# Performance work log

Measured on AMD Instinct MI355X. Metric: run time of the kernel, lower is better.

## Reference

```python
import jax, jax.numpy as jnp
import numpy as np

GROUP_SIZE = 64
SCALING = 1.0  # lora_alpha / r = 16 / 16
# bitsandbytes NF4 codebook (16 normal-float levels)
NF4_CODE = jnp.array([
    -1.0, -0.6961928009986877, -0.5250730514526367, -0.39491748809814453,
    -0.28444138169288635, -0.18477343022823334, -0.09105003625154495, 0.0,
    0.07958029955625534, 0.16093020141124725, 0.24611230194568634,
    0.33791524171829224, 0.44070982933044434, 0.5626170039176941,
    0.7229568362236023, 1.0], dtype=jnp.float32)

IN_F, OUT_F, R, TOKENS = 4096, 11008, 16, 32


def setup_inputs() -> dict:
    key = jax.random.key(0)
    k0, k1, k2, k3, k4 = jax.random.split(key, 5)
    x = jax.random.normal(k0, (TOKENS, IN_F), dtype=jnp.float32)
    # each byte packs two 4-bit NF4 indices (high nibble first)
    packed_weight = jax.random.randint(k1, (OUT_F * IN_F // 2,), 0, 256, dtype=jnp.int32)
    # per-group absmax scales (positive)
    scales = jax.random.uniform(k2, (OUT_F * IN_F // GROUP_SIZE,), dtype=jnp.float32,
                                minval=0.005, maxval=0.05)
    lora_A = jax.random.normal(k3, (R, IN_F), dtype=jnp.float32) * 0.02
    lora_B = jax.random.normal(k4, (OUT_F, R), dtype=jnp.float32) * 0.02
    return {"x": x, "packed_weight": packed_weight, "scales": scales,
            "lora_A": lora_A, "lora_B": lora_B}


def _dequant_nf4(packed_weight, scales):
    hi = packed_weight // 16          # first nibble
    lo = packed_weight % 16           # second nibble
    idx = jnp.stack([hi, lo], axis=-1).reshape(-1)          # [out*in]
    w = NF4_CODE[idx].reshape(-1, GROUP_SIZE) * scales[:, None]
    return w.reshape(OUT_F, IN_F)                            # [out, in]


def reference(x, packed_weight, scales, lora_A, lora_B):
    W = _dequant_nf4(packed_weight, scales)
    base = x @ W.T                                           # [tokens, out]
    lora = (x @ lora_A.T) @ lora_B.T                         # low-rank update
    return base + SCALING * lora
```

## Files before the change

kernel.cpp:

```cpp
#include <hip/hip_runtime.h>
#include <hip/hip_bf16.h>

#define IN_F 4096
#define OUT_F 11008
#define TOKENS 32
#define RANK 16
#define KSPLIT 8
#define KSLICE (IN_F / KSPLIT)
#define XPAD 520

typedef unsigned short u16;
typedef __attribute__((ext_vector_type(8))) short bf16x8;
typedef __attribute__((ext_vector_type(4))) float f32x4;

__device__ const float NF4_d[16] = {
    -1.0f, -0.6961928009986877f, -0.5250730514526367f, -0.39491748809814453f,
    -0.28444138169288635f, -0.18477343022823334f, -0.09105003625154495f, 0.0f,
    0.07958029955625534f, 0.16093020141124725f, 0.24611230194568634f,
    0.33791524171829224f, 0.44070982933044434f, 0.5626170039176941f,
    0.7229568362236023f, 1.0f};

static __device__ __forceinline__ unsigned pk2(float a, float b) {
    __hip_bfloat162 h = __float22bfloat162_rn(make_float2(a, b));
    unsigned u;
    __builtin_memcpy(&u, &h, 4);
    return u;
}

__global__ void prep(const float* __restrict__ x, const float* __restrict__ A,
                     u16* __restrict__ xbf, float* __restrict__ xa) {
    __shared__ float red[256];
    if (blockIdx.x >= 512) {
        int i4 = (blockIdx.x - 512) * 256 + threadIdx.x;
        float4 v = ((const float4*)x)[i4];
        uint2 o;
        o.x = pk2(v.x, v.y);
        o.y = pk2(v.z, v.w);
        ((uint2*)xbf)[i4] = o;
        return;
    }
    int b = blockIdx.x;
    int t = b >> 4, r = b & 15;
    const float4* xr = (const float4*)(x + t * IN_F);
    const float4* ar = (const float4*)(A + r * IN_F);
    float s = 0.f;
    for (int c = 0; c < 4; ++c) {
        int j = c * 256 + threadIdx.x;
        float4 xv = xr[j], av = ar[j];
        s += xv.x * av.x + xv.y * av.y + xv.z * av.z + xv.w * av.w;
    }
    red[threadIdx.x] = s;
    __syncthreads();
    for (int st = 128; st > 0; st >>= 1) {
        if (threadIdx.x < st) red[threadIdx.x] += red[threadIdx.x + st];
        __syncthreads();
    }
    if (threadIdx.x == 0) xa[b] = red[0];
}

__global__ void lora_out(const float* __restrict__ xa, const float* __restrict__ B,
                         float* __restrict__ out) {
    int idx = blockIdx.x * 256 + threadIdx.x;
    int t = idx / OUT_F;
    int o = idx - t * OUT_F;
    const float4* br = (const float4*)(B + o * RANK);
    const float4* xr = (const float4*)(xa + t * RANK);
    float acc = 0.f;
    for (int c = 0; c < 4; ++c) {
        float4 bv = br[c], xv = xr[c];
        acc += bv.x * xv.x + bv.y * xv.y + bv.z * xv.z + bv.w * xv.w;
    }
    out[idx] = acc;
}

__global__ __launch_bounds__(256) void qlora_main(const int* __restrict__ packed,
                                                  const float* __restrict__ scales,
                                                  const u16* __restrict__ xbf,
                                                  float* __restrict__ out) {
    __shared__ u16 xs[32 * XPAD];
    __shared__ float2 tbl[256];
    __shared__ float sl[64 * 9];
    const int tid = threadIdx.x;
    const int kbase = blockIdx.y * KSLICE;
    const int obase = blockIdx.x * 64;

    tbl[tid] = make_float2(NF4_d[tid >> 4], NF4_d[tid & 15]);

    {
        int r = tid >> 3, g = tid & 7;
        int g0 = (kbase >> 6);
        sl[r * 9 + g] = scales[(obase + r) * 64 + g0 + g];
        sl[(r + 32) * 9 + g] = scales[(obase + r + 32) * 64 + g0 + g];
    }

    for (int it = 0; it < 8; ++it) {
        int row = it * 4 + (tid >> 6);
        int c8 = tid & 63;
        *(uint4*)(xs + row * XPAD + c8 * 8) =
            *(const uint4*)(xbf + row * IN_F + kbase + c8 * 8);
    }
    __syncthreads();

    const int lane = tid & 63;
    const int wv = tid >> 6;
    const int n = lane & 15;
    const int q = lane >> 4;
    const int o = obase + wv * 16 + n;

    const int4* pp = (const int4*)(packed + o * 2048 + (kbase >> 1)) + q;

    f32x4 acc0 = {0.f, 0.f, 0.f, 0.f};
    f32x4 acc1 = {0.f, 0.f, 0.f, 0.f};
    const u16* xr0 = xs + n * XPAD + q * 8;
    const u16* xr1 = xs + (n + 16) * XPAD + q * 8;
    const float* slp = sl + (wv * 16 + n) * 9;

    int4 c0 = pp[0];
    int4 c1 = pp[4];

#pragma unroll
    for (int s = 0; s < 16; s += 2) {
        int4 n0 = c0, n1 = c1;
        if (s + 2 < 16) {
            n0 = pp[(s + 2) * 4];
            n1 = pp[(s + 3) * 4];
        }
        float sc = slp[s >> 1];

        {
            float2 d0 = tbl[c0.x & 255];
            float2 d1 = tbl[c0.y & 255];
            float2 d2 = tbl[c0.z & 255];
            float2 d3 = tbl[c0.w & 255];
            uint4 bu;
            bu.x = pk2(d0.x * sc, d0.y * sc);
            bu.y = pk2(d1.x * sc, d1.y * sc);
            bu.z = pk2(d2.x * sc, d2.y * sc);
            bu.w = pk2(d3.x * sc, d3.y * sc);
            bf16x8 bfrag;
            __builtin_memcpy(&bfrag, &bu, 16);
            bf16x8 a0 = *(const bf16x8*)(xr0 + s * 32);
            bf16x8 a1 = *(const bf16x8*)(xr1 + s * 32);
            acc0 = __builtin_amdgcn_mfma_f32_16x16x32_bf16(a0, bfrag, acc0, 0, 0, 0);
            acc1 = __builtin_amdgcn_mfma_f32_16x16x32_bf16(a1, bfrag, acc1, 0, 0, 0);
        }
        {
            float2 d0 = tbl[c1.x & 255];
            float2 d1 = tbl[c1.y & 255];
            float2 d2 = tbl[c1.z & 255];
            float2 d3 = tbl[c1.w & 255];
            uint4 bu;
            bu.x = pk2(d0.x * sc, d0.y * sc);
            bu.y = pk2(d1.x * sc, d1.y * sc);
            bu.z = pk2(d2.x * sc, d2.y * sc);
            bu.w = pk2(d3.x * sc, d3.y * sc);
            bf16x8 bfrag;
            __builtin_memcpy(&bfrag, &bu, 16);
            bf16x8 a0 = *(const bf16x8*)(xr0 + (s + 1) * 32);
            bf16x8 a1 = *(const bf16x8*)(xr1 + (s + 1) * 32);
            acc0 = __builtin_amdgcn_mfma_f32_16x16x32_bf16(a0, bfrag, acc0, 0, 0, 0);
            acc1 = __builtin_amdgcn_mfma_f32_16x16x32_bf16(a1, bfrag, acc1, 0, 0, 0);
        }
        c0 = n0;
        c1 = n1;
    }

    for (int r = 0; r < 4; ++r) {
        int t = q * 4 + r;
        atomicAdd(out + t * OUT_F + o, acc0[r]);
        atomicAdd(out + (t + 16) * OUT_F + o, acc1[r]);
    }
}

extern "C" void kernel_launch(void* const* d_in, const int* in_sizes, int n_in,
                              void* d_out, int out_size, void* d_ws, size_t ws_size,
                              hipStream_t stream) {
    const float* x = (const float*)d_in[0];
    const int* packed = (const int*)d_in[1];
    const float* scales = (const float*)d_in[2];
    const float* lora_A = (const float*)d_in[3];
    const float* lora_B = (const float*)d_in[4];
    float* out = (float*)d_out;

    u16* xbf = (u16*)d_ws;
    float* xa = (float*)((char*)d_ws + TOKENS * IN_F * 2);

    prep<<<640, 256, 0, stream>>>(x, lora_A, xbf, xa);
    lora_out<<<(TOKENS * OUT_F) / 256, 256, 0, stream>>>(xa, lora_B, out);
    qlora_main<<<dim3(OUT_F / 64, KSPLIT), 256, 0, stream>>>(packed, scales, xbf, out);
}
```

Measured before the change: 155.6 us.

## Replace atomic split-K with partial buffers, bpermute NF4 lookup, drop LDS staging

The main kernel now writes per-K-slice partial sums to a workspace buffer instead of issuing atomicAdd to the output, and a new reduce kernel sums the four partials and adds the LoRA term. The K split drops from 8 to 4. NF4 decode now uses ds_bpermute on a per-lane codebook register instead of a shared-memory pair table. The x tile is read directly from global memory rather than staged in LDS. The intent is to remove atomic traffic and shared-memory setup and barriers, at the cost of extra partial-buffer writes and reads and fewer blocks in flight.

```diff
diff --git a/kernel.cpp b/kernel.cpp
--- a/kernel.cpp
+++ b/kernel.cpp
@@ -5,9 +5,9 @@
 #define OUT_F 11008
 #define TOKENS 32
 #define RANK 16
-#define KSPLIT 8
+#define KSPLIT 4
 #define KSLICE (IN_F / KSPLIT)
-#define XPAD 520
+#define OUT_ELEMS (TOKENS * OUT_F)
 
 typedef unsigned short u16;
 typedef __attribute__((ext_vector_type(8))) short bf16x8;
@@ -25,6 +25,14 @@
     unsigned u;
     __builtin_memcpy(&u, &h, 4);
     return u;
+}
+
+static __device__ __forceinline__ unsigned dq_byte(int b, int codei, float sc) {
+    int ih = (b >> 2) & 0x3C;
+    int il = (b << 2) & 0x3C;
+    float h = __int_as_float(__builtin_amdgcn_ds_bpermute(ih, codei));
+    float l = __int_as_float(__builtin_amdgcn_ds_bpermute(il, codei));
+    return pk2(h * sc, l * sc);
 }
 
 __global__ void prep(const float* __restrict__ x, const float* __restrict__ A,
@@ -58,11 +66,87 @@
     if (threadIdx.x == 0) xa[b] = red[0];
 }
 
-__global__ void lora_out(const float* __restrict__ xa, const float* __restrict__ B,
-                         float* __restrict__ out) {
+__global__ __launch_bounds__(256) void qlora_part(const int* __restrict__ packed,
+                                                  const float* __restrict__ scales,
+                                                  const u16* __restrict__ xbf,
+                                                  float* __restrict__ part) {
+    const int tid = threadIdx.x;
+    const int lane = tid & 63;
+    const int wv = tid >> 6;
+    const int n = lane & 15;
+    const int q = lane >> 4;
+    const int kbase = blockIdx.y * KSLICE;
+    const int o = blockIdx.x * 64 + wv * 16 + n;
+
+    const int codei = __float_as_int(NF4_d[lane & 15]);
+
+    const int4* ppq = (const int4*)(packed + o * 2048 + (kbase >> 1)) + q;
+    const u16* xq0 = xbf + n * IN_F + kbase + q * 8;
+    const u16* xq1 = xq0 + 16 * IN_F;
+    const float* sg = scales + o * 64 + (kbase >> 6);
+
+    f32x4 acc0 = {0.f, 0.f, 0.f, 0.f};
+    f32x4 acc1 = {0.f, 0.f, 0.f, 0.f};
+
+    int4 c0 = ppq[0];
+    int4 c1 = ppq[4];
+
+#pragma unroll
+    for (int s = 0; s < 32; s += 2) {
+        int4 n0 = c0, n1 = c1;
+        if (s + 2 < 32) {
+            n0 = ppq[(s + 2) * 4];
+            n1 = ppq[(s + 3) * 4];
+        }
+        float sc = sg[s >> 1];
+
+        {
+            uint4 bu;
+            bu.x = dq_byte(c0.x, codei, sc);
+            bu.y = dq_byte(c0.y, codei, sc);
+            bu.z = dq_byte(c0.z, codei, sc);
+            bu.w = dq_byte(c0.w, codei, sc);
+            bf16x8 bfrag;
+            __builtin_memcpy(&bfrag, &bu, 16);
+            bf16x8 a0 = *(const bf16x8*)(xq0 + s * 32);
+            bf16x8 a1 = *(const bf16x8*)(xq1 + s * 32);
+            acc0 = __builtin_amdgcn_mfma_f32_16x16x32_bf16(a0, bfrag, acc0, 0, 0, 0);
+            acc1 = __builtin_amdgcn_mfma_f32_16x16x32_bf16(a1, bfrag, acc1, 0, 0, 0);
+        }
+        {
+            uint4 bu;
+            bu.x = dq_byte(c1.x, codei, sc);
+            bu.y = dq_byte(c1.y, codei, sc);
+            bu.z = dq_byte(c1.z, codei, sc);
+            bu.w = dq_byte(c1.w, codei, sc);
+            bf16x8 bfrag;
+            __builtin_memcpy(&bfrag, &bu, 16);
+            bf16x8 a0 = *(const bf16x8*)(xq0 + (s + 1) * 32);
+            bf16x8 a1 = *(const bf16x8*)(xq1 + (s + 1) * 32);
+            acc0 = __builtin_amdgcn_mfma_f32_16x16x32_bf16(a0, bfrag, acc0, 0, 0, 0);
+            acc1 = __builtin_amdgcn_mfma_f32_16x16x32_bf16(a1, bfrag, acc1, 0, 0, 0);
+        }
+        c0 = n0;
+        c1 = n1;
+    }
+
+    float* pb = part + blockIdx.y * OUT_ELEMS + o;
+    for (int r = 0; r < 4; ++r) {
+        int t = q * 4 + r;
+        pb[t * OUT_F] = acc0[r];
+        pb[(t + 16) * OUT_F] = acc1[r];
+    }
+}
+
+__global__ void reduce_lora(const float* __restrict__ part,
+                            const float* __restrict__ xa,
+                            const float* __restrict__ B,
+                            float* __restrict__ out) {
     int idx = blockIdx.x * 256 + threadIdx.x;
     int t = idx / OUT_F;
     int o = idx - t * OUT_F;
+    float s = part[idx] + part[idx + OUT_ELEMS] + part[idx + 2 * OUT_ELEMS] +
+              part[idx + 3 * OUT_ELEMS];
     const float4* br = (const float4*)(B + o * RANK);
     const float4* xr = (const float4*)(xa + t * RANK);
     float acc = 0.f;
@@ -70,106 +154,7 @@
         float4 bv = br[c], xv = xr[c];
         acc += bv.x * xv.x + bv.y * xv.y + bv.z * xv.z + bv.w * xv.w;
     }
-    out[idx] = acc;
-}
-
-__global__ __launch_bounds__(256) void qlora_main(const int* __restrict__ packed,
-                                                  const float* __restrict__ scales,
-                                                  const u16* __restrict__ xbf,
-                                                  float* __restrict__ out) {
-    __shared__ u16 xs[32 * XPAD];
-    __shared__ float2 tbl[256];
-    __shared__ float sl[64 * 9];
-    const int tid = threadIdx.x;
-    const int kbase = blockIdx.y * KSLICE;
-    const int obase = blockIdx.x * 64;
-
-    tbl[tid] = make_float2(NF4_d[tid >> 4], NF4_d[tid & 15]);
-
-    {
-        int r = tid >> 3, g = tid & 7;
-        int g0 = (kbase >> 6);
-        sl[r * 9 + g] = scales[(obase + r) * 64 + g0 + g];
-        sl[(r + 32) * 9 + g] = scales[(obase + r + 32) * 64 + g0 + g];
-    }
-
-    for (int it = 0; it < 8; ++it) {
-        int row = it * 4 + (tid >> 6);
-        int c8 = tid & 63;
-        *(uint4*)(xs + row * XPAD + c8 * 8) =
-            *(const uint4*)(xbf + row * IN_F + kbase + c8 * 8);
-    }
-    __syncthreads();
-
-    const int lane = tid & 63;
-    const int wv = tid >> 6;
-    const int n = lane & 15;
-    const int q = lane >> 4;
-    const int o = obase + wv * 16 + n;
-
-    const int4* pp = (const int4*)(packed + o * 2048 + (kbase >> 1)) + q;
-
-    f32x4 acc0 = {0.f, 0.f, 0.f, 0.f};
-    f32x4 acc1 = {0.f, 0.f, 0.f, 0.f};
-    const u16* xr0 = xs + n * XPAD + q * 8;
-    const u16* xr1 = xs + (n + 16) * XPAD + q * 8;
-    const float* slp = sl + (wv * 16 + n) * 9;
-
-    int4 c0 = pp[0];
-    int4 c1 = pp[4];
-
-#pragma unroll
-    for (int s = 0; s < 16; s += 2) {
-        int4 n0 = c0, n1 = c1;
-        if (s + 2 < 16) {
-            n0 = pp[(s + 2) * 4];
-            n1 = pp[(s + 3) * 4];
-        }
-        float sc = slp[s >> 1];
-
-        {
-            float2 d0 = tbl[c0.x & 255];
-            float2 d1 = tbl[c0.y & 255];
-            float2 d2 = tbl[c0.z & 255];
-            float2 d3 = tbl[c0.w & 255];
-            uint4 bu;
-            bu.x = pk2(d0.x * sc, d0.y * sc);
-            bu.y = pk2(d1.x * sc, d1.y * sc);
-            bu.z = pk2(d2.x * sc, d2.y * sc);
-            bu.w = pk2(d3.x * sc, d3.y * sc);
-            bf16x8 bfrag;
-            __builtin_memcpy(&bfrag, &bu, 16);
-            bf16x8 a0 = *(const bf16x8*)(xr0 + s * 32);
-            bf16x8 a1 = *(const bf16x8*)(xr1 + s * 32);
-            acc0 = __builtin_amdgcn_mfma_f32_16x16x32_bf16(a0, bfrag, acc0, 0, 0, 0);
-            acc1 = __builtin_amdgcn_mfma_f32_16x16x32_bf16(a1, bfrag, acc1, 0, 0, 0);
-        }
-        {
-            float2 d0 = tbl[c1.x & 255];
-            float2 d1 = tbl[c1.y & 255];
-            float2 d2 = tbl[c1.z & 255];
-            float2 d3 = tbl[c1.w & 255];
-            uint4 bu;
-            bu.x = pk2(d0.x * sc, d0.y * sc);
-            bu.y = pk2(d1.x * sc, d1.y * sc);
-            bu.z = pk2(d2.x * sc, d2.y * sc);
-            bu.w = pk2(d3.x * sc, d3.y * sc);
-            bf16x8 bfrag;
-            __builtin_memcpy(&bfrag, &bu, 16);
-            bf16x8 a0 = *(const bf16x8*)(xr0 + (s + 1) * 32);
-            bf16x8 a1 = *(const bf16x8*)(xr1 + (s + 1) * 32);
-            acc0 = __builtin_amdgcn_mfma_f32_16x16x32_bf16(a0, bfrag, acc0, 0, 0, 0);
-            acc1 = __builtin_amdgcn_mfma_f32_16x16x32_bf16(a1, bfrag, acc1, 0, 0, 0);
-        }
-        c0 = n0;
-        c1 = n1;
-    }
-
-    for (int r = 0; r < 4; ++r) {
-        int t = q * 4 + r;
-        atomicAdd(out + t * OUT_F + o, acc0[r]);
-        atomicAdd(out + (t + 16) * OUT_F + o, acc1[r]);
-    }
+    out[idx] = s + acc;
 }
 
 extern "C" void kernel_launch(void* const* d_in, const int* in_sizes, int n_in,
@@ -183,9 +168,10 @@
     float* out = (float*)d_out;
 
     u16* xbf = (u16*)d_ws;
-    float* xa = (float*)((char*)d_ws + TOKENS * IN_F * 2);
+    float* xa = (float*)((char*)d_ws + 262144);
+    float* part = (float*)((char*)d_ws + 264192);
 
     prep<<<640, 256, 0, stream>>>(x, lora_A, xbf, xa);
-    lora_out<<<(TOKENS * OUT_F) / 256, 256, 0, stream>>>(xa, lora_B, out);
-    qlora_main<<<dim3(OUT_F / 64, KSPLIT), 256, 0, stream>>>(packed, scales, xbf, out);
+    qlora_part<<<dim3(OUT_F / 64, KSPLIT), 256, 0, stream>>>(packed, scales, xbf, part);
+    reduce_lora<<<OUT_ELEMS / 256, 256, 0, stream>>>(part, xa, lora_B, out);
 }
```

After: 163.8 us. 1.05x slower.

## Prefetch packed weights before LDS staging, deepen pipeline, shrink NF4 table, vectorize LoRA

Applied to the files above, without the earlier changes.

The main kernel now issues its first four packed-weight loads and the per-row scale loads before staging x into shared memory. This hides global latency behind the LDS fill, and the main loop keeps four chunks in flight instead of two. The NF4 pair table is packed as bf16 pairs in 32-bit words, and the scale LDS array is replaced by direct float4 register loads. The LoRA output kernel computes four outputs per thread with vectorized stores, and launch_bounds adds an occupancy hint. The cost is higher register pressure from the deeper prefetch.

```diff
diff --git a/kernel.cpp b/kernel.cpp
--- a/kernel.cpp
+++ b/kernel.cpp
@@ -60,38 +60,52 @@
 
 __global__ void lora_out(const float* __restrict__ xa, const float* __restrict__ B,
                          float* __restrict__ out) {
-    int idx = blockIdx.x * 256 + threadIdx.x;
-    int t = idx / OUT_F;
-    int o = idx - t * OUT_F;
-    const float4* br = (const float4*)(B + o * RANK);
+    int idx4 = blockIdx.x * 256 + threadIdx.x;
+    int t = idx4 / (OUT_F / 4);
+    int o4 = idx4 - t * (OUT_F / 4);
+    const float4* br = (const float4*)(B + o4 * 4 * RANK);
     const float4* xr = (const float4*)(xa + t * RANK);
-    float acc = 0.f;
-    for (int c = 0; c < 4; ++c) {
-        float4 bv = br[c], xv = xr[c];
-        acc += bv.x * xv.x + bv.y * xv.y + bv.z * xv.z + bv.w * xv.w;
+    float4 xv0 = xr[0], xv1 = xr[1], xv2 = xr[2], xv3 = xr[3];
+    float res[4];
+#pragma unroll
+    for (int j = 0; j < 4; ++j) {
+        float4 b0 = br[j * 4 + 0], b1 = br[j * 4 + 1];
+        float4 b2 = br[j * 4 + 2], b3 = br[j * 4 + 3];
+        res[j] = b0.x * xv0.x + b0.y * xv0.y + b0.z * xv0.z + b0.w * xv0.w +
+                 b1.x * xv1.x + b1.y * xv1.y + b1.z * xv1.z + b1.w * xv1.w +
+                 b2.x * xv2.x + b2.y * xv2.y + b2.z * xv2.z + b2.w * xv2.w +
+                 b3.x * xv3.x + b3.y * xv3.y + b3.z * xv3.z + b3.w * xv3.w;
     }
-    out[idx] = acc;
+    float4 r4 = make_float4(res[0], res[1], res[2], res[3]);
+    *(float4*)(out + t * OUT_F + o4 * 4) = r4;
 }
 
-__global__ __launch_bounds__(256) void qlora_main(const int* __restrict__ packed,
-                                                  const float* __restrict__ scales,
-                                                  const u16* __restrict__ xbf,
-                                                  float* __restrict__ out) {
+__global__ __launch_bounds__(256, 4) void qlora_main(const int* __restrict__ packed,
+                                                     const float* __restrict__ scales,
+                                                     const u16* __restrict__ xbf,
+                                                     float* __restrict__ out) {
     __shared__ u16 xs[32 * XPAD];
-    __shared__ float2 tbl[256];
-    __shared__ float sl[64 * 9];
+    __shared__ unsigned tbl[256];
     const int tid = threadIdx.x;
     const int kbase = blockIdx.y * KSLICE;
     const int obase = blockIdx.x * 64;
 
-    tbl[tid] = make_float2(NF4_d[tid >> 4], NF4_d[tid & 15]);
+    const int lane = tid & 63;
+    const int wv = tid >> 6;
+    const int n = lane & 15;
+    const int q = lane >> 4;
+    const int o = obase + wv * 16 + n;
 
-    {
-        int r = tid >> 3, g = tid & 7;
-        int g0 = (kbase >> 6);
-        sl[r * 9 + g] = scales[(obase + r) * 64 + g0 + g];
-        sl[(r + 32) * 9 + g] = scales[(obase + r + 32) * 64 + g0 + g];
-    }
+    const int4* ppq = (const int4*)(packed + o * 2048 + (kbase >> 1)) + q;
+    int4 P0 = ppq[0];
+    int4 P1 = ppq[4];
+    int4 P2 = ppq[8];
+    int4 P3 = ppq[12];
+
+    const float4* sp = (const float4*)(scales + o * 64 + (kbase >> 6));
+    float4 sA = sp[0], sB = sp[1];
+
+    tbl[tid] = pk2(NF4_d[tid & 15], NF4_d[tid >> 4]);
 
     for (int it = 0; it < 8; ++it) {
         int row = it * 4 + (tid >> 6);
@@ -101,68 +115,51 @@
     }
     __syncthreads();
 
-    const int lane = tid & 63;
-    const int wv = tid >> 6;
-    const int n = lane & 15;
-    const int q = lane >> 4;
-    const int o = obase + wv * 16 + n;
-
-    const int4* pp = (const int4*)(packed + o * 2048 + (kbase >> 1)) + q;
-
     f32x4 acc0 = {0.f, 0.f, 0.f, 0.f};
     f32x4 acc1 = {0.f, 0.f, 0.f, 0.f};
     const u16* xr0 = xs + n * XPAD + q * 8;
     const u16* xr1 = xs + (n + 16) * XPAD + q * 8;
-    const float* slp = sl + (wv * 16 + n) * 9;
 
-    int4 c0 = pp[0];
-    int4 c1 = pp[4];
+    int4 P[4] = {P0, P1, P2, P3};
+    const float scr[8] = {sA.x, sA.y, sA.z, sA.w, sB.x, sB.y, sB.z, sB.w};
 
 #pragma unroll
-    for (int s = 0; s < 16; s += 2) {
-        int4 n0 = c0, n1 = c1;
-        if (s + 2 < 16) {
-            n0 = pp[(s + 2) * 4];
-            n1 = pp[(s + 3) * 4];
-        }
-        float sc = slp[s >> 1];
+    for (int s = 0; s < 16; ++s) {
+        int4 cur = P[s & 3];
+        if (s + 4 < 16) P[s & 3] = ppq[(s + 4) * 4];
+        float sc = scr[s >> 1];
 
+        unsigned u0 = tbl[cur.x & 255];
+        unsigned u1 = tbl[cur.y & 255];
+        unsigned u2 = tbl[cur.z & 255];
+        unsigned u3 = tbl[cur.w & 255];
+        uint4 bu;
         {
-            float2 d0 = tbl[c0.x & 255];
-            float2 d1 = tbl[c0.y & 255];
-            float2 d2 = tbl[c0.z & 255];
-            float2 d3 = tbl[c0.w & 255];
-            uint4 bu;
-            bu.x = pk2(d0.x * sc, d0.y * sc);
-            bu.y = pk2(d1.x * sc, d1.y * sc);
-            bu.z = pk2(d2.x * sc, d2.y * sc);
-            bu.w = pk2(d3.x * sc, d3.y * sc);
-            bf16x8 bfrag;
-            __builtin_memcpy(&bfrag, &bu, 16);
-            bf16x8 a0 = *(const bf16x8*)(xr0 + s * 32);
-            bf16x8 a1 = *(const bf16x8*)(xr1 + s * 32);
-            acc0 = __builtin_amdgcn_mfma_f32_16x16x32_bf16(a0, bfrag, acc0, 0, 0, 0);
-            acc1 = __builtin_amdgcn_mfma_f32_16x16x32_bf16(a1, bfrag, acc1, 0, 0, 0);
+            float h = __int_as_float(u0 & 0xFFFF0000u);
+            float l = __int_as_float(u0 << 16);
+            bu.x = pk2(h * sc, l * sc);
         }
         {
-            float2 d0 = tbl[c1.x & 255];
-            float2 d1 = tbl[c1.y & 255];
-            float2 d2 = tbl[c1.z & 255];
-            float2 d3 = tbl[c1.w & 255];
-            uint4 bu;
-            bu.x = pk2(d0.x * sc, d0.y * sc);
-            bu.y = pk2(d1.x * sc, d1.y * sc);
-            bu.z = pk2(d2.x * sc, d2.y * sc);
-            bu.w = pk2(d3.x * sc, d3.y * sc);
-            bf16x8 bfrag;
-            __builtin_memcpy(&bfrag, &bu, 16);
-            bf16x8 a0 = *(const bf16x8*)(xr0 + (s + 1) * 32);
-            bf16x8 a1 = *(const bf16x8*)(xr1 + (s + 1) * 32);
-            acc0 = __builtin_amdgcn_mfma_f32_16x16x32_bf16(a0, bfrag, acc0, 0, 0, 0);
-            acc1 = __builtin_amdgcn_mfma_f32_16x16x32_bf16(a1, bfrag, acc1, 0, 0, 0);
+            float h = __int_as_float(u1 & 0xFFFF0000u);
+            float l = __int_as_float(u1 << 16);
+            bu.y = pk2(h * sc, l * sc);
         }
-        c0 = n0;
-        c1 = n1;
+        {
+            float h = __int_as_float(u2 & 0xFFFF0000u);
+            float l = __int_as_float(u2 << 16);
+            bu.z = pk2(h * sc, l * sc);
+        }
+        {
+            float h = __int_as_float(u3 & 0xFFFF0000u);
+            float l = __int_as_float(u3 << 16);
+            bu.w = pk2(h * sc, l * sc);
+        }
+        bf16x8 bfrag;
+        __builtin_memcpy(&bfrag, &bu, 16);
+        bf16x8 a0 = *(const bf16x8*)(xr0 + s * 32);
+        bf16x8 a1 = *(const bf16x8*)(xr1 + s * 32);
+        acc0 = __builtin_amdgcn_mfma_f32_16x16x32_bf16(a0, bfrag, acc0, 0, 0, 0);
+        acc1 = __builtin_amdgcn_mfma_f32_16x16x32_bf16(a1, bfrag, acc1, 0, 0, 0);
     }
 
     for (int r = 0; r < 4; ++r) {
@@ -183,9 +180,9 @@
     float* out = (float*)d_out;
 
     u16* xbf = (u16*)d_ws;
-    float* xa = (float*)((char*)d_ws + TOKENS * IN_F * 2);
+    float* xa = (float*)((char*)d_ws + 262144);
 
     prep<<<640, 256, 0, stream>>>(x, lora_A, xbf, xa);
-    lora_out<<<(TOKENS * OUT_F) / 256, 256, 0, stream>>>(xa, lora_B, out);
+    lora_out<<<(TOKENS * OUT_F / 4) / 256, 256, 0, stream>>>(xa, lora_B, out);
     qlora_main<<<dim3(OUT_F / 64, KSPLIT), 256, 0, stream>>>(packed, scales, xbf, out);
 }
```

New measurement: 158.5 us. Within noise of the previous version (+1.9%).
